# Performance work log

Hardware: AMD Instinct MI355X
Metric: run time of the kernel (lower is better)

## Reference

```python
import jax, jax.numpy as jnp
import numpy as np


def setup_inputs() -> dict:
    key = jax.random.key(0)
    k1, k2, k3 = jax.random.split(key, 3)
    B, C, N, Ht, Wt = 2, 16, 512, 64, 64
    Ho, Wo = 1024, 1024
    x = jax.random.normal(k1, (B, C, N, Ht, Wt), dtype=jnp.float32)
    quad_idx = jax.random.randint(k2, (Ho, Wo), 0, N, dtype=jnp.int64)
    tex_uv = jax.random.uniform(k3, (Ho, Wo, 2), dtype=jnp.float32)
    return {"x": x, "quad_idx": quad_idx, "tex_uv": tex_uv}


def reference(x, quad_idx, tex_uv):
    """Per-pixel texture gather + bilinear UV sampling.

    x:        [B, C, N, Ht, Wt] atlas of N textures
    quad_idx: [Ho, Wo] int texture index per output pixel
    tex_uv:   [Ho, Wo, 2] normalized (u, v) in [0, 1]
    returns:  [B, C, Ho, Wo]
    """
    B, C, N, Ht, Wt = x.shape
    Ho, Wo = quad_idx.shape

    # map normalized uv -> pixel coordinates
    u = tex_uv[..., 0] * (Wt - 1)  # [Ho, Wo]
    v = tex_uv[..., 1] * (Ht - 1)

    x0f = jnp.floor(u)
    y0f = jnp.floor(v)
    wu = u - x0f  # bilinear weights
    wv = v - y0f

    x0 = jnp.clip(x0f.astype(jnp.int32), 0, Wt - 1)
    y0 = jnp.clip(y0f.astype(jnp.int32), 0, Ht - 1)
    x1 = jnp.clip(x0 + 1, 0, Wt - 1)
    y1 = jnp.clip(y0 + 1, 0, Ht - 1)

    # flatten texture atlas so one gather covers (texture, y, x)
    flat = x.reshape(B, C, N * Ht * Wt)
    base = quad_idx.astype(jnp.int32) * (Ht * Wt)  # [Ho, Wo]

    def gather(yi, xi):
        idx = (base + yi * Wt + xi).reshape(-1)            # [Ho*Wo]
        return jnp.take(flat, idx, axis=2).reshape(B, C, Ho, Wo)

    g00 = gather(y0, x0)
    g01 = gather(y0, x1)
    g10 = gather(y1, x0)
    g11 = gather(y1, x1)

    wu = wu[None, None]  # [1, 1, Ho, Wo]
    wv = wv[None, None]
    out = ((1.0 - wv) * ((1.0 - wu) * g00 + wu * g01)
           + wv * ((1.0 - wu) * g10 + wu * g11))
    return out
```

## Files before the change

### kernel.cpp

```cpp
#include <hip/hip_runtime.h>

#define HT 64
#define WT 64
#define NTEX 512
#define HO 1024
#define WO 1024
#define NCH 32
#define SLAB (HT * WT)
#define NPIX (HO * WO)
#define PXB 4096
#define NBLK (NPIX / PXB)

typedef float    f32x4 __attribute__((ext_vector_type(4)));
typedef unsigned u32x4 __attribute__((ext_vector_type(4)));

#define WS_BASE   0
#define WS_PART   16384
#define WS_BBASE  (16384 + 512 * 1024)
#define MB (1u << 20)
#define WS_RANK   ((size_t)16384 + 1 * MB)
#define WS_METAB  ((size_t)16384 + 5 * MB)
#define WS_CMP    ((size_t)16384 + 13 * MB)
#define WS_METAS  ((size_t)16384 + 1 * MB)
#define WS_NEED_SMALL ((size_t)16384 + 10 * (size_t)MB)
#define WS_NEED_BIG   ((size_t)16384 + 141 * (size_t)MB)

__global__ __launch_bounds__(256) void k_hist(const int* __restrict__ qi,
                                              unsigned* __restrict__ partial) {
    __shared__ unsigned h[NTEX];
    for (int i = threadIdx.x; i < NTEX; i += 256) h[i] = 0;
    __syncthreads();
    const int p0 = blockIdx.x * PXB;
    for (int k = threadIdx.x; k < PXB; k += 256)
        atomicAdd(&h[qi[p0 + k]], 1u);
    __syncthreads();
    unsigned* row = partial + (size_t)blockIdx.x * NTEX;
    for (int i = threadIdx.x; i < NTEX; i += 256) row[i] = h[i];
}

__global__ __launch_bounds__(512) void k_scan(const unsigned* __restrict__ partial,
                                              unsigned* __restrict__ base,
                                              unsigned* __restrict__ blockbase) {
    __shared__ unsigned t[NTEX];
    const int i = threadIdx.x;
    unsigned total = 0;
    for (int b = 0; b < NBLK; ++b)
        total += partial[(size_t)b * NTEX + i];
    t[i] = total;
    __syncthreads();
    for (int s = 1; s < NTEX; s <<= 1) {
        unsigned v = (i >= s) ? t[i - s] : 0u;
        __syncthreads();
        t[i] += v;
        __syncthreads();
    }
    const unsigned excl = t[i] - total;
    base[i] = excl;
    if (i == NTEX - 1) base[NTEX] = t[i];
    unsigned run = excl;
    for (int b = 0; b < NBLK; ++b) {
        blockbase[(size_t)b * NTEX + i] = run;
        run += partial[(size_t)b * NTEX + i];
    }
}

__global__ __launch_bounds__(256) void k_meta(const int* __restrict__ qi,
                                              const float* __restrict__ uvp,
                                              const unsigned* __restrict__ blockbase,
                                              uint2* __restrict__ meta,
                                              unsigned* __restrict__ rank_of) {
    __shared__ unsigned lbase[NTEX];
    __shared__ unsigned lcount[NTEX];
    const int p0 = blockIdx.x * PXB;
    const unsigned* row = blockbase + (size_t)blockIdx.x * NTEX;
    for (int i = threadIdx.x; i < NTEX; i += 256) {
        lbase[i] = row[i];
        lcount[i] = 0;
    }
    __syncthreads();

    for (int k = threadIdx.x; k < PXB; k += 256) {
        const int pix = p0 + k;
        const int n = qi[pix];
        const float2 uv = reinterpret_cast<const float2*>(uvp)[pix];

        const float u = uv.x * (float)(WT - 1);
        const float v = uv.y * (float)(HT - 1);
        int x0 = (int)floorf(u);
        int y0 = (int)floorf(v);
        x0 = min(max(x0, 0), WT - 2);
        y0 = min(max(y0, 0), HT - 2);
        const float wu = u - (float)x0;
        const float wv = v - (float)y0;

        const unsigned off  = (unsigned)(y0 * WT + x0);
        const unsigned key  = ((unsigned)pix << 12) | off;
        const unsigned wu16 = (unsigned)__float2int_rn(wu * 65535.0f);
        const unsigned wv16 = (unsigned)__float2int_rn(wv * 65535.0f);

        const unsigned rank = lbase[n] + atomicAdd(&lcount[n], 1u);
        meta[rank] = make_uint2(key, wu16 | (wv16 << 16));
        if (rank_of) rank_of[pix] = rank;
    }
}

__global__ __launch_bounds__(512) void k_gather4(const float* __restrict__ x,
                                                 const unsigned* __restrict__ base,
                                                 const uint2* __restrict__ meta,
                                                 float* __restrict__ compact) {
    __shared__ float s[4 * SLAB];
    const int b = blockIdx.x;
    const int n = b & 511;
    const int cg = b >> 9;
    const int tid = threadIdx.x;

    #pragma unroll
    for (int ch = 0; ch < 4; ++ch) {
        const f32x4* __restrict__ src = reinterpret_cast<const f32x4*>(
            x + ((size_t)(cg * 4 + ch) * NTEX + n) * SLAB);
        f32x4* d = reinterpret_cast<f32x4*>(s + ch * SLAB);
        d[tid]       = src[tid];
        d[tid + 512] = src[tid + 512];
    }
    __syncthreads();

    const unsigned lo = base[n];
    const unsigned cnt = base[n + 1] - lo;
    const uint2* __restrict__ m = meta + lo;
    f32x4* __restrict__ cc =
        reinterpret_cast<f32x4*>(compact) + (size_t)cg * NPIX + lo;

    for (unsigned j = tid; j < cnt; j += 512) {
        const uint2 r = m[j];
        const unsigned off = r.x & 4095u;
        const float wu = (float)(r.y & 65535u) * (1.0f / 65535.0f);
        const float wv = (float)(r.y >> 16) * (1.0f / 65535.0f);

        f32x4 o;
        #pragma unroll
        for (int ch = 0; ch < 4; ++ch) {
            const float* __restrict__ sc = s + ch * SLAB + off;
            const float g00 = sc[0];
            const float g01 = sc[1];
            const float g10 = sc[WT];
            const float g11 = sc[WT + 1];
            const float top = g00 + wu * (g01 - g00);
            const float bot = g10 + wu * (g11 - g10);
            o[ch] = top + wv * (bot - top);
        }
        __builtin_nontemporal_store(o, cc + j);
    }
}

__global__ __launch_bounds__(256) void k_scatter4(const unsigned* __restrict__ rank_of,
                                                  const float* __restrict__ compact,
                                                  float* __restrict__ out) {
    const int t = threadIdx.x;
    const int P = blockIdx.x * 1024;
    const u32x4 r4 =
        *reinterpret_cast<const u32x4*>(rank_of + P + 4 * t);
    const f32x4* __restrict__ cp = reinterpret_cast<const f32x4*>(compact);

    f32x4 v[8][4];
    #pragma unroll
    for (int cg = 0; cg < 8; ++cg) {
        #pragma unroll
        for (int k = 0; k < 4; ++k)
            v[cg][k] = cp[(size_t)cg * NPIX + r4[k]];
    }

    float* __restrict__ o = out + P + 4 * t;
    #pragma unroll
    for (int cg = 0; cg < 8; ++cg) {
        #pragma unroll
        for (int kc = 0; kc < 4; ++kc) {
            f32x4 w;
            w.x = v[cg][0][kc];
            w.y = v[cg][1][kc];
            w.z = v[cg][2][kc];
            w.w = v[cg][3][kc];
            __builtin_nontemporal_store(w,
                reinterpret_cast<f32x4*>(o + (size_t)(cg * 4 + kc) * NPIX));
        }
    }
}

__global__ __launch_bounds__(256) void k_main(const float* __restrict__ x,
                                              const unsigned* __restrict__ base,
                                              const uint2* __restrict__ meta,
                                              float* __restrict__ out) {
    __shared__ float s[SLAB];

    const int b = blockIdx.x;
    const int xcd = b & 7;
    const int i = b >> 3;
    const int cgrp = i >> 9;
    const int n = i & 511;
    const int c = cgrp * 8 + xcd;

    const f32x4* __restrict__ slab4 =
        reinterpret_cast<const f32x4*>(x + ((size_t)c * NTEX + n) * SLAB);
    f32x4* s4 = reinterpret_cast<f32x4*>(s);
    #pragma unroll
    for (int j = 0; j < 4; ++j)
        s4[threadIdx.x + 256 * j] = slab4[threadIdx.x + 256 * j];
    __syncthreads();

    const unsigned lo = base[n];
    const unsigned cnt = base[n + 1] - lo;
    const uint2* __restrict__ m = meta + lo;
    float* __restrict__ o = out + (size_t)c * NPIX;

    for (unsigned j = threadIdx.x; j < cnt; j += 256) {
        const uint2 r = m[j];
        const unsigned off = r.x & 4095u;
        const unsigned pix = r.x >> 12;
        const float wu = (float)(r.y & 65535u) * (1.0f / 65535.0f);
        const float wv = (float)(r.y >> 16) * (1.0f / 65535.0f);

        const float g00 = s[off];
        const float g01 = s[off + 1];
        const float g10 = s[off + WT];
        const float g11 = s[off + WT + 1];

        const float top = g00 + wu * (g01 - g00);
        const float bot = g10 + wu * (g11 - g10);
        o[pix] = top + wv * (bot - top);
    }
}

__global__ __launch_bounds__(256) void k_direct(const float* __restrict__ x,
                                                const int* __restrict__ quad_idx,
                                                const float* __restrict__ tex_uv,
                                                float* __restrict__ out) {
    const int pix = blockIdx.x * blockDim.x + threadIdx.x;
    const int chunk = blockIdx.y;
    const int n = quad_idx[pix];
    const float2 uv = reinterpret_cast<const float2*>(tex_uv)[pix];
    const float u = uv.x * (float)(WT - 1);
    const float v = uv.y * (float)(HT - 1);
    int x0 = (int)floorf(u), y0 = (int)floorf(v);
    x0 = min(max(x0, 0), WT - 2);
    y0 = min(max(y0, 0), HT - 2);
    const float wu = u - (float)x0, wv = v - (float)y0;
    const float w00 = (1.f - wu) * (1.f - wv), w01 = wu * (1.f - wv);
    const float w10 = (1.f - wu) * wv, w11 = wu * wv;
    const int off0 = n * SLAB + y0 * WT + x0, off1 = off0 + WT;
    const float* p = x + (size_t)chunk * 8 * NTEX * SLAB;
    float* o = out + (size_t)chunk * 8 * NPIX + pix;
    #pragma unroll
    for (int ch = 0; ch < 8; ++ch) {
        float2 r0, r1;
        __builtin_memcpy(&r0, p + off0, 8);
        __builtin_memcpy(&r1, p + off1, 8);
        o[0] = w00 * r0.x + w01 * r0.y + w10 * r1.x + w11 * r1.y;
        p += (size_t)NTEX * SLAB;
        o += NPIX;
    }
}

extern "C" void kernel_launch(void* const* d_in, const int* in_sizes, int n_in,
                              void* d_out, int out_size, void* d_ws, size_t ws_size,
                              hipStream_t stream) {
    const float* x        = (const float*)d_in[0];
    const int*   quad_idx = (const int*)d_in[1];
    const float* tex_uv   = (const float*)d_in[2];
    float*       out      = (float*)d_out;
    char* ws = (char*)d_ws;

    if (ws_size >= WS_NEED_BIG) {
        unsigned* base      = (unsigned*)(ws + WS_BASE);
        unsigned* partial   = (unsigned*)(ws + WS_PART);
        unsigned* blockbase = (unsigned*)(ws + WS_BBASE);
        unsigned* rank_of   = (unsigned*)(ws + WS_RANK);
        uint2*    meta      = (uint2*)(ws + WS_METAB);
        float*    compact   = (float*)(ws + WS_CMP);

        k_hist<<<NBLK, 256, 0, stream>>>(quad_idx, partial);
        k_scan<<<1, 512, 0, stream>>>(partial, base, blockbase);
        k_meta<<<NBLK, 256, 0, stream>>>(quad_idx, tex_uv, blockbase,
                                         meta, rank_of);
        k_gather4<<<NTEX * 8, 512, 0, stream>>>(x, base, meta, compact);
        k_scatter4<<<NPIX / 1024, 256, 0, stream>>>(rank_of, compact, out);
    } else if (ws_size >= WS_NEED_SMALL) {
        unsigned* base      = (unsigned*)(ws + WS_BASE);
        unsigned* partial   = (unsigned*)(ws + WS_PART);
        unsigned* blockbase = (unsigned*)(ws + WS_BBASE);
        uint2*    meta      = (uint2*)(ws + WS_METAS);

        k_hist<<<NBLK, 256, 0, stream>>>(quad_idx, partial);
        k_scan<<<1, 512, 0, stream>>>(partial, base, blockbase);
        k_meta<<<NBLK, 256, 0, stream>>>(quad_idx, tex_uv, blockbase,
                                         meta, (unsigned*)nullptr);
        k_main<<<NTEX * NCH, 256, 0, stream>>>(x, base, meta, out);
    } else {
        dim3 grid(NPIX / 256, 4);
        k_direct<<<grid, 256, 0, stream>>>(x, quad_idx, tex_uv, out);
    }
}
```

Baseline: 575.1 us.

## Widen gather to 8-channel groups and compute block prefix bases in k_meta

The gather kernel now stages 8 channels of a texture slab in shared memory (128 KB) instead of 4 and writes 32-byte f32x8 records per pixel. The scatter then reads 4 channel groups of 8 instead of 8 groups of 4, with fewer, wider random reads. Separately, the single-block scan no longer writes the per-block base table; each k_meta block sums the partial histograms of earlier blocks itself. This removes a serial 256-iteration loop in one block but adds redundant partial reads that grow with block index, and the larger shared footprint lowers gather occupancy.

```diff
diff --git a/kernel.cpp b/kernel.cpp
--- a/kernel.cpp
+++ b/kernel.cpp
@@ -12,11 +12,11 @@
 #define NBLK (NPIX / PXB)
 
 typedef float    f32x4 __attribute__((ext_vector_type(4)));
+typedef float    f32x8 __attribute__((ext_vector_type(8)));
 typedef unsigned u32x4 __attribute__((ext_vector_type(4)));
 
 #define WS_BASE   0
 #define WS_PART   16384
-#define WS_BBASE  (16384 + 512 * 1024)
 #define MB (1u << 20)
 #define WS_RANK   ((size_t)16384 + 1 * MB)
 #define WS_METAB  ((size_t)16384 + 5 * MB)
@@ -39,8 +39,7 @@
 }
 
 __global__ __launch_bounds__(512) void k_scan(const unsigned* __restrict__ partial,
-                                              unsigned* __restrict__ base,
-                                              unsigned* __restrict__ blockbase) {
+                                              unsigned* __restrict__ base) {
     __shared__ unsigned t[NTEX];
     const int i = threadIdx.x;
     unsigned total = 0;
@@ -54,32 +53,34 @@
         t[i] += v;
         __syncthreads();
     }
-    const unsigned excl = t[i] - total;
-    base[i] = excl;
+    base[i] = t[i] - total;
     if (i == NTEX - 1) base[NTEX] = t[i];
-    unsigned run = excl;
-    for (int b = 0; b < NBLK; ++b) {
-        blockbase[(size_t)b * NTEX + i] = run;
-        run += partial[(size_t)b * NTEX + i];
-    }
 }
 
 __global__ __launch_bounds__(256) void k_meta(const int* __restrict__ qi,
                                               const float* __restrict__ uvp,
-                                              const unsigned* __restrict__ blockbase,
+                                              const unsigned* __restrict__ partial,
+                                              const unsigned* __restrict__ base,
                                               uint2* __restrict__ meta,
                                               unsigned* __restrict__ rank_of) {
     __shared__ unsigned lbase[NTEX];
     __shared__ unsigned lcount[NTEX];
+    const int tid = threadIdx.x;
     const int p0 = blockIdx.x * PXB;
-    const unsigned* row = blockbase + (size_t)blockIdx.x * NTEX;
-    for (int i = threadIdx.x; i < NTEX; i += 256) {
-        lbase[i] = row[i];
-        lcount[i] = 0;
-    }
-    __syncthreads();
-
-    for (int k = threadIdx.x; k < PXB; k += 256) {
+
+    unsigned acc0 = 0, acc1 = 0;
+    for (int b2 = 0; b2 < blockIdx.x; ++b2) {
+        const unsigned* row = partial + (size_t)b2 * NTEX;
+        acc0 += row[tid];
+        acc1 += row[tid + 256];
+    }
+    lbase[tid]       = base[tid] + acc0;
+    lbase[tid + 256] = base[tid + 256] + acc1;
+    lcount[tid] = 0;
+    lcount[tid + 256] = 0;
+    __syncthreads();
+
+    for (int k = tid; k < PXB; k += 256) {
         const int pix = p0 + k;
         const int n = qi[pix];
         const float2 uv = reinterpret_cast<const float2*>(uvp)[pix];
@@ -104,20 +105,20 @@
     }
 }
 
-__global__ __launch_bounds__(512) void k_gather4(const float* __restrict__ x,
+__global__ __launch_bounds__(512) void k_gather8(const float* __restrict__ x,
                                                  const unsigned* __restrict__ base,
                                                  const uint2* __restrict__ meta,
                                                  float* __restrict__ compact) {
-    __shared__ float s[4 * SLAB];
+    __shared__ float s[8 * SLAB];
     const int b = blockIdx.x;
     const int n = b & 511;
     const int cg = b >> 9;
     const int tid = threadIdx.x;
 
     #pragma unroll
-    for (int ch = 0; ch < 4; ++ch) {
+    for (int ch = 0; ch < 8; ++ch) {
         const f32x4* __restrict__ src = reinterpret_cast<const f32x4*>(
-            x + ((size_t)(cg * 4 + ch) * NTEX + n) * SLAB);
+            x + ((size_t)(cg * 8 + ch) * NTEX + n) * SLAB);
         f32x4* d = reinterpret_cast<f32x4*>(s + ch * SLAB);
         d[tid]       = src[tid];
         d[tid + 512] = src[tid + 512];
@@ -127,8 +128,7 @@
     const unsigned lo = base[n];
     const unsigned cnt = base[n + 1] - lo;
     const uint2* __restrict__ m = meta + lo;
-    f32x4* __restrict__ cc =
-        reinterpret_cast<f32x4*>(compact) + (size_t)cg * NPIX + lo;
+    float* __restrict__ cc = compact + ((size_t)cg * NPIX + lo) * 8;
 
     for (unsigned j = tid; j < cnt; j += 512) {
         const uint2 r = m[j];
@@ -136,9 +136,9 @@
         const float wu = (float)(r.y & 65535u) * (1.0f / 65535.0f);
         const float wv = (float)(r.y >> 16) * (1.0f / 65535.0f);
 
-        f32x4 o;
+        f32x8 o;
         #pragma unroll
-        for (int ch = 0; ch < 4; ++ch) {
+        for (int ch = 0; ch < 8; ++ch) {
             const float* __restrict__ sc = s + ch * SLAB + off;
             const float g00 = sc[0];
             const float g01 = sc[1];
@@ -148,39 +148,35 @@
             const float bot = g10 + wu * (g11 - g10);
             o[ch] = top + wv * (bot - top);
         }
-        __builtin_nontemporal_store(o, cc + j);
-    }
-}
-
-__global__ __launch_bounds__(256) void k_scatter4(const unsigned* __restrict__ rank_of,
-                                                  const float* __restrict__ compact,
-                                                  float* __restrict__ out) {
+        __builtin_nontemporal_store(o,
+            reinterpret_cast<f32x8*>(cc + (size_t)j * 8));
+    }
+}
+
+__global__ __launch_bounds__(256) void k_scatter(const unsigned* __restrict__ rank_of,
+                                                 const float* __restrict__ compact,
+                                                 float* __restrict__ out) {
     const int t = threadIdx.x;
     const int P = blockIdx.x * 1024;
-    const u32x4 r4 =
-        *reinterpret_cast<const u32x4*>(rank_of + P + 4 * t);
-    const f32x4* __restrict__ cp = reinterpret_cast<const f32x4*>(compact);
-
-    f32x4 v[8][4];
-    #pragma unroll
-    for (int cg = 0; cg < 8; ++cg) {
+    const u32x4 r4 = *reinterpret_cast<const u32x4*>(rank_of + P + 4 * t);
+    const f32x8* __restrict__ cp = reinterpret_cast<const f32x8*>(compact);
+    float* __restrict__ o = out + P + 4 * t;
+
+    #pragma unroll
+    for (int cg = 0; cg < 4; ++cg) {
+        f32x8 a0 = cp[(size_t)cg * NPIX + r4[0]];
+        f32x8 a1 = cp[(size_t)cg * NPIX + r4[1]];
+        f32x8 a2 = cp[(size_t)cg * NPIX + r4[2]];
+        f32x8 a3 = cp[(size_t)cg * NPIX + r4[3]];
         #pragma unroll
-        for (int k = 0; k < 4; ++k)
-            v[cg][k] = cp[(size_t)cg * NPIX + r4[k]];
-    }
-
-    float* __restrict__ o = out + P + 4 * t;
-    #pragma unroll
-    for (int cg = 0; cg < 8; ++cg) {
-        #pragma unroll
-        for (int kc = 0; kc < 4; ++kc) {
+        for (int ch = 0; ch < 8; ++ch) {
             f32x4 w;
-            w.x = v[cg][0][kc];
-            w.y = v[cg][1][kc];
-            w.z = v[cg][2][kc];
-            w.w = v[cg][3][kc];
+            w.x = a0[ch];
+            w.y = a1[ch];
+            w.z = a2[ch];
+            w.w = a3[ch];
             __builtin_nontemporal_store(w,
-                reinterpret_cast<f32x4*>(o + (size_t)(cg * 4 + kc) * NPIX));
+                reinterpret_cast<f32x4*>(o + (size_t)(cg * 8 + ch) * NPIX));
         }
     }
 }
@@ -269,28 +265,26 @@
     char* ws = (char*)d_ws;
 
     if (ws_size >= WS_NEED_BIG) {
-        unsigned* base      = (unsigned*)(ws + WS_BASE);
-        unsigned* partial   = (unsigned*)(ws + WS_PART);
-        unsigned* blockbase = (unsigned*)(ws + WS_BBASE);
-        unsigned* rank_of   = (unsigned*)(ws + WS_RANK);
-        uint2*    meta      = (uint2*)(ws + WS_METAB);
-        float*    compact   = (float*)(ws + WS_CMP);
+        unsigned* base    = (unsigned*)(ws + WS_BASE);
+        unsigned* partial = (unsigned*)(ws + WS_PART);
+        unsigned* rank_of = (unsigned*)(ws + WS_RANK);
+        uint2*    meta    = (uint2*)(ws + WS_METAB);
+        float*    compact = (float*)(ws + WS_CMP);
 
         k_hist<<<NBLK, 256, 0, stream>>>(quad_idx, partial);
-        k_scan<<<1, 512, 0, stream>>>(partial, base, blockbase);
-        k_meta<<<NBLK, 256, 0, stream>>>(quad_idx, tex_uv, blockbase,
+        k_scan<<<1, 512, 0, stream>>>(partial, base);
+        k_meta<<<NBLK, 256, 0, stream>>>(quad_idx, tex_uv, partial, base,
                                          meta, rank_of);
-        k_gather4<<<NTEX * 8, 512, 0, stream>>>(x, base, meta, compact);
-        k_scatter4<<<NPIX / 1024, 256, 0, stream>>>(rank_of, compact, out);
+        k_gather8<<<NTEX * 4, 512, 0, stream>>>(x, base, meta, compact);
+        k_scatter<<<NPIX / 1024, 256, 0, stream>>>(rank_of, compact, out);
     } else if (ws_size >= WS_NEED_SMALL) {
-        unsigned* base      = (unsigned*)(ws + WS_BASE);
-        unsigned* partial   = (unsigned*)(ws + WS_PART);
-        unsigned* blockbase = (unsigned*)(ws + WS_BBASE);
-        uint2*    meta      = (uint2*)(ws + WS_METAS);
+        unsigned* base    = (unsigned*)(ws + WS_BASE);
+        unsigned* partial = (unsigned*)(ws + WS_PART);
+        uint2*    meta    = (uint2*)(ws + WS_METAS);
 
         k_hist<<<NBLK, 256, 0, stream>>>(quad_idx, partial);
-        k_scan<<<1, 512, 0, stream>>>(partial, base, blockbase);
-        k_meta<<<NBLK, 256, 0, stream>>>(quad_idx, tex_uv, blockbase,
+        k_scan<<<1, 512, 0, stream>>>(partial, base);
+        k_meta<<<NBLK, 256, 0, stream>>>(quad_idx, tex_uv, partial, base,
                                          meta, (unsigned*)nullptr);
         k_main<<<NTEX * NCH, 256, 0, stream>>>(x, base, meta, out);
     } else {
```

After: 562.4 us. 2.2% less time.
